# Kernel optimization log

Hardware: AMD Instinct MI355X
Metric: run time of the kernel (lower is better)

## Reference

```python
import jax, jax.numpy as jnp
import numpy as np

B = 65536
L_IN = 1024
DS_FACTOR = 4  # 1024 -> 256 per DownsampleLY so cat gives 512


def fwht(x):
    """Fast Walsh-Hadamard transform over last dim, orthonormal (1/sqrt(n)) scaling."""
    n = x.shape[-1]
    lead = x.shape[:-1]
    h = 1
    while h < n:
        xr = x.reshape(lead + (n // (2 * h), 2, h))
        a = xr[..., 0, :]
        b = xr[..., 1, :]
        x = jnp.stack((a + b, a - b), axis=-2).reshape(lead + (n,))
        h *= 2
    return x * jnp.asarray(1.0 / np.sqrt(n), x.dtype)


def setup_inputs() -> dict:
    key = jax.random.key(0)
    ks = jax.random.split(key, 20)
    s = 0.05  # small init scale for numerical stability
    inp = {
        "x": jax.random.normal(ks[0], (B, L_IN), jnp.float32),
        # learnable downsample taps (factor-4 weighted pooling)
        "dw1": jax.random.normal(ks[1], (DS_FACTOR,), jnp.float32) * 0.25 + 0.25,
        "dw2": jax.random.normal(ks[2], (DS_FACTOR,), jnp.float32) * 0.25 + 0.25,
        # encoder: 512->512->128->64
        "eW1": jax.random.normal(ks[3], (512, 512), jnp.float32) * s,
        "eb1": jnp.zeros((512,), jnp.float32),
        "eW2": jax.random.normal(ks[4], (512, 128), jnp.float32) * s,
        "eb2": jnp.zeros((128,), jnp.float32),
        "eW3": jax.random.normal(ks[5], (128, 64), jnp.float32) * s,
        "eb3": jnp.zeros((64,), jnp.float32),
        # WHT1D channel mix (in=out=1 -> scalar scale + bias)
        "w1c": jnp.ones((), jnp.float32),
        "w1b": jnp.zeros((), jnp.float32),
        # decoder: 64->128->32
        "dW1": jax.random.normal(ks[6], (64, 128), jnp.float32) * s,
        "db1": jnp.zeros((128,), jnp.float32),
        "dW2": jax.random.normal(ks[7], (128, 32), jnp.float32) * s,
        "db2": jnp.zeros((32,), jnp.float32),
        "w2c": jnp.ones((), jnp.float32),
        "w2b": jnp.zeros((), jnp.float32),
        # proj: 32->32
        "pW": jax.random.normal(ks[8], (32, 32), jnp.float32) * s,
        "pb": jnp.zeros((32,), jnp.float32),
    }
    return inp


def reference(x, dw1, dw2, eW1, eb1, eW2, eb2, eW3, eb3, w1c, w1b,
              dW1, db1, dW2, db2, w2c, w2b, pW, pb):
    b = x.shape[0]
    xr = x.reshape(b, L_IN // DS_FACTOR, DS_FACTOR)  # (B, 256, 4)
    R = jnp.einsum('btk,k->bt', xr, dw1)             # (B, 256)
    Z = jnp.einsum('btk,k->bt', xr, dw2)             # (B, 256)
    h = jnp.concatenate((R, Z), axis=1)              # (B, 512)
    # encoder MLP
    h = jax.nn.relu(h @ eW1 + eb1)
    h = jax.nn.relu(h @ eW2 + eb2)
    h = h @ eW3 + eb3                                # (B, 64)
    # WHT1D(64) with 1x1 channel mix
    h = fwht(h) * w1c + w1b
    # decoder MLP
    h = jax.nn.relu(h @ dW1 + db1)
    h = h @ dW2 + db2                                # (B, 32)
    # WHT1D(32)
    h = fwht(h) * w2c + w2b
    # final projection -> (B, 32): [:,:16] real, [:,16:] imag
    return h @ pW + pb
```

## Files before the change

### kernel.cpp

```cpp
#include <hip/hip_runtime.h>

typedef _Float16 f16x8 __attribute__((ext_vector_type(8)));
typedef float f32x4 __attribute__((ext_vector_type(4)));

#define MFMA16(a, b, c) __builtin_amdgcn_mfma_f32_16x16x32_f16(a, b, c, 0, 0, 0)

#define OFF_W1   0u
#define OFF_W2   524288u
#define OFF_W3   655360u
#define OFF_W4   671744u
#define OFF_W5   688128u
#define OFF_W6   696320u
#define OFF_DB1  698368u
#define OFF_PB   698880u

__device__ inline void packw(int local, int N, const float* __restrict__ W,
                             _Float16* __restrict__ dst) {
  int j = local & 7;
  int lane = (local >> 3) & 63;
  int fi = local >> 9;
  int NF = N >> 4;
  int nf = fi % NF;
  int kk = fi / NF;
  int k = kk * 32 + ((lane >> 4) << 3) + j;
  int n = (nf << 4) + (lane & 15);
  dst[local] = (_Float16)W[k * N + n];
}

__device__ inline void packh(int local, int N, int K, const float* __restrict__ W,
                             _Float16* __restrict__ dst, float scale) {
  int j = local & 7;
  int lane = (local >> 3) & 63;
  int fi = local >> 9;
  int NF = N >> 4;
  int nf = fi % NF;
  int kk = fi / NF;
  int k = kk * 32 + ((lane >> 4) << 3) + j;
  int n = (nf << 4) + (lane & 15);
  float s = 0.f;
  for (int m = 0; m < K; ++m) {
    float v = W[m * N + n];
    s += (__popc(k & m) & 1) ? -v : v;
  }
  dst[local] = (_Float16)(s * scale);
}

extern "C" __global__ __launch_bounds__(256) void prep_kernel(
    const float* __restrict__ eW1, const float* __restrict__ eW2,
    const float* __restrict__ eW3, const float* __restrict__ dW1,
    const float* __restrict__ dW2, const float* __restrict__ pW,
    const float* __restrict__ w1c, const float* __restrict__ w1b,
    const float* __restrict__ w2c, const float* __restrict__ w2b,
    const float* __restrict__ db1, const float* __restrict__ pb,
    char* __restrict__ ws) {
  int idx = blockIdx.x * 256 + threadIdx.x;
  if (idx < 262144) {
    packw(idx, 512, eW1, (_Float16*)(ws + OFF_W1));
  } else if (idx < 327680) {
    packw(idx - 262144, 128, eW2, (_Float16*)(ws + OFF_W2));
  } else if (idx < 335872) {
    packw(idx - 327680, 64, eW3, (_Float16*)(ws + OFF_W3));
  } else if (idx < 344064) {
    packh(idx - 335872, 128, 64, dW1, (_Float16*)(ws + OFF_W4), w1c[0] * 0.125f);
  } else if (idx < 348160) {
    packw(idx - 344064, 32, dW2, (_Float16*)(ws + OFF_W5));
  } else if (idx < 349184) {
    packh(idx - 348160, 32, 32, pW, (_Float16*)(ws + OFF_W6),
          w2c[0] * 0.17677669529663687f);
  } else if (idx < 349312) {
    int n = idx - 349184;
    float s = 0.f;
    for (int m = 0; m < 64; ++m) s += dW1[m * 128 + n];
    ((float*)(ws + OFF_DB1))[n] = db1[n] + w1b[0] * s;
  } else if (idx < 349344) {
    int n = idx - 349312;
    float s = 0.f;
    for (int m = 0; m < 32; ++m) s += pW[m * 32 + n];
    ((float*)(ws + OFF_PB))[n] = pb[n] + w2b[0] * s;
  }
}

__device__ inline int hidx(int row, int col, int nu) {
  int u = (col >> 3) ^ ((row & 7) & (nu - 1));
  return row * (nu << 3) + (u << 3) + (col & 7);
}

__device__ inline f16x8 afrag(const _Float16* h, int row, int col, int nu) {
  return *(const f16x8*)(h + hidx(row, col, nu));
}

template <int KK, int NUIN, int NUOUT, bool RELU, int MT>
__device__ inline void layerN(const _Float16* hin, _Float16* hout,
                              const f16x8* __restrict__ Wp,
                              const float* __restrict__ bias, int NFtot, int m0,
                              int nf0, int lane, int g, int rr) {
  f32x4 acc[MT];
#pragma unroll
  for (int m = 0; m < MT; ++m) acc[m] = (f32x4){0.f, 0.f, 0.f, 0.f};
#pragma unroll
  for (int kk = 0; kk < KK; ++kk) {
    f16x8 b = Wp[(kk * NFtot + nf0) * 64 + lane];
#pragma unroll
    for (int m = 0; m < MT; ++m) {
      f16x8 a = afrag(hin, (m0 + m) * 16 + rr, kk * 32 + g * 8, NUIN);
      acc[m] = MFMA16(a, b, acc[m]);
    }
  }
  const int n = nf0 * 16 + rr;
  const float bv = bias[n];
#pragma unroll
  for (int m = 0; m < MT; ++m) {
#pragma unroll
    for (int i = 0; i < 4; ++i) {
      float v = acc[m][i] + bv;
      if (RELU) v = fmaxf(v, 0.f);
      hout[hidx((m0 + m) * 16 + g * 4 + i, n, NUOUT)] = (_Float16)v;
    }
  }
}

#define LDC(C)                                              \
  do {                                                      \
    const float4* p0_ = xrow0 + (C) * 32;                   \
    const float4* p1_ = xrow1 + (C) * 32;                   \
    q0 = p0_[e];  q1 = p0_[e + 8];  q2 = p0_[e + 16];  q3 = p0_[e + 24]; \
    q4 = p1_[e];  q5 = p1_[e + 8];  q6 = p1_[e + 16];  q7 = p1_[e + 24]; \
  } while (0)

#define DOTR(V) (_Float16)((V).x * d10 + (V).y * d11 + (V).z * d12 + (V).w * d13)
#define DOTZ(V) (_Float16)((V).x * d20 + (V).y * d21 + (V).z * d22 + (V).w * d23)

#define CONVQ2(V, ROW, JJ, SR, SZ)                                \
  do {                                                            \
    int ix_ = (ROW) * 32 + ((((JJ) ^ ((ROW) & 3))) << 3) + e;     \
    (SR)[ix_] = DOTR(V);                                          \
    (SZ)[ix_] = DOTZ(V);                                          \
  } while (0)

#define CONVC(SR, SZ)                                             \
  do {                                                            \
    CONVQ2(q0, r8, 0, SR, SZ); CONVQ2(q1, r8, 1, SR, SZ);         \
    CONVQ2(q2, r8, 2, SR, SZ); CONVQ2(q3, r8, 3, SR, SZ);         \
    CONVQ2(q4, r8 + 64, 0, SR, SZ); CONVQ2(q5, r8 + 64, 1, SR, SZ); \
    CONVQ2(q6, r8 + 64, 2, SR, SZ); CONVQ2(q7, r8 + 64, 3, SR, SZ); \
  } while (0)

#define GRID 512

extern "C" __global__ __launch_bounds__(512)
__attribute__((amdgpu_waves_per_eu(2, 2))) void fused_kernel(
    const float* __restrict__ x, const float* __restrict__ dw1,
    const float* __restrict__ dw2, const float* __restrict__ eb1,
    const float* __restrict__ eb2, const float* __restrict__ eb3,
    const float* __restrict__ db2, const char* __restrict__ ws,
    float* __restrict__ out) {
  __shared__ __align__(16) _Float16 LDS[73728];
  _Float16* const h1 = LDS;
  _Float16* const h2 = LDS;
  _Float16* const h4 = LDS + 16384;
  _Float16* const h5 = LDS + 40960;
  _Float16* const h3 = LDS + 65536;
  _Float16* const s0R = LDS + 49152;
  _Float16* const s0Z = LDS + 53248;
  _Float16* const s1R = LDS + 57344;
  _Float16* const s1Z = LDS + 61440;

  const int tid = threadIdx.x;
  const int wg = blockIdx.x;
  const int lane = tid & 63;
  const int w = tid >> 6;
  const int g = lane >> 4;
  const int rr = lane & 15;
  const int r8 = tid >> 3;
  const int e = tid & 7;

  const float d10 = dw1[0], d11 = dw1[1], d12 = dw1[2], d13 = dw1[3];
  const float d20 = dw2[0], d21 = dw2[1], d22 = dw2[2], d23 = dw2[3];

  const f16x8* __restrict__ W1 = (const f16x8*)(ws + OFF_W1);
  const f16x8* __restrict__ W2 = (const f16x8*)(ws + OFF_W2);
  const f16x8* __restrict__ W3 = (const f16x8*)(ws + OFF_W3);
  const f16x8* __restrict__ W4 = (const f16x8*)(ws + OFF_W4);
  const f16x8* __restrict__ W5 = (const f16x8*)(ws + OFF_W5);
  const f16x8* __restrict__ W6 = (const f16x8*)(ws + OFF_W6);
  const float* __restrict__ db1p = (const float*)(ws + OFF_DB1);
  const float* __restrict__ pbp = (const float*)(ws + OFF_PB);

  const float4* __restrict__ xrow0 =
      (const float4*)x + ((size_t)wg * 128 + r8) * 256;
  const float4* __restrict__ xrow1 = xrow0 + (size_t)64 * 256;

  float4 q0, q1, q2, q3, q4, q5, q6, q7;

  LDC(0);
  CONVC(s0R, s0Z);
  __syncthreads();

  f32x4 acc[8][4];
#pragma unroll
  for (int m = 0; m < 8; ++m)
#pragma unroll
    for (int n = 0; n < 4; ++n) acc[m][n] = (f32x4){0.f, 0.f, 0.f, 0.f};

  for (int c = 0; c < 8; ++c) {
    if (c < 7) LDC(c + 1);
    const _Float16* sRp = (c & 1) ? s1R : s0R;
    const _Float16* sZp = (c & 1) ? s1Z : s0Z;
#pragma unroll
    for (int S = 0; S < 2; ++S) {
      const _Float16* sl = S ? sZp : sRp;
      const int kk = S ? (8 + c) : c;
      f16x8 a0 = afrag(sl, rr, g * 8, 4);
      f16x8 a1 = afrag(sl, 16 + rr, g * 8, 4);
      f16x8 a2 = afrag(sl, 32 + rr, g * 8, 4);
      f16x8 a3 = afrag(sl, 48 + rr, g * 8, 4);
      f16x8 a4 = afrag(sl, 64 + rr, g * 8, 4);
      f16x8 a5 = afrag(sl, 80 + rr, g * 8, 4);
      f16x8 a6 = afrag(sl, 96 + rr, g * 8, 4);
      f16x8 a7 = afrag(sl, 112 + rr, g * 8, 4);
#pragma unroll
      for (int nf = 0; nf < 4; ++nf) {
        f16x8 bb = W1[(kk * 32 + w * 4 + nf) * 64 + lane];
        acc[0][nf] = MFMA16(a0, bb, acc[0][nf]);
        acc[1][nf] = MFMA16(a1, bb, acc[1][nf]);
        acc[2][nf] = MFMA16(a2, bb, acc[2][nf]);
        acc[3][nf] = MFMA16(a3, bb, acc[3][nf]);
        acc[4][nf] = MFMA16(a4, bb, acc[4][nf]);
        acc[5][nf] = MFMA16(a5, bb, acc[5][nf]);
        acc[6][nf] = MFMA16(a6, bb, acc[6][nf]);
        acc[7][nf] = MFMA16(a7, bb, acc[7][nf]);
      }
    }
    if (c < 7) {
      _Float16* dR = (c & 1) ? s0R : s1R;
      _Float16* dZ = (c & 1) ? s0Z : s1Z;
      CONVC(dR, dZ);
    }
    __syncthreads();
  }

#pragma unroll
  for (int mt = 0; mt < 8; ++mt) {
#pragma unroll
    for (int nf = 0; nf < 4; ++nf) {
      const int n = (w * 4 + nf) * 16 + rr;
      const float bv = eb1[n];
#pragma unroll
      for (int i = 0; i < 4; ++i) {
        float v = fmaxf(acc[mt][nf][i] + bv, 0.f);
        h1[hidx(mt * 16 + g * 4 + i, n, 64)] = (_Float16)v;
      }
    }
  }
  __syncthreads();

  {
    f32x4 acc2[8];
#pragma unroll
    for (int m = 0; m < 8; ++m) acc2[m] = (f32x4){0.f, 0.f, 0.f, 0.f};
#pragma unroll
    for (int kk = 0; kk < 16; ++kk) {
      f16x8 b2 = W2[(kk * 8 + w) * 64 + lane];
#pragma unroll
      for (int m = 0; m < 8; ++m) {
        f16x8 a = afrag(h1, m * 16 + rr, kk * 32 + g * 8, 64);
        acc2[m] = MFMA16(a, b2, acc2[m]);
      }
    }
    const float bv2 = eb2[w * 16 + rr];
    __syncthreads();
#pragma unroll
    for (int m = 0; m < 8; ++m) {
#pragma unroll
      for (int i = 0; i < 4; ++i) {
        float v = fmaxf(acc2[m][i] + bv2, 0.f);
        h2[hidx(m * 16 + g * 4 + i, w * 16 + rr, 16)] = (_Float16)v;
      }
    }
  }
  __syncthreads();

  layerN<4, 16, 8, false, 4>(h2, h3, W3, eb3, 4, (w >> 2) * 4, w & 3, lane, g, rr);
  __syncthreads();
  layerN<2, 8, 16, true, 8>(h3, h4, W4, db1p, 8, 0, w, lane, g, rr);
  __syncthreads();
  layerN<4, 16, 4, false, 2>(h4, h5, W5, db2, 2, (w >> 1) * 2, w & 1, lane, g, rr);
  __syncthreads();

  {
    const int m5 = (w >> 1) * 2;
    const int nf5 = w & 1;
    const int n = nf5 * 16 + rr;
    const float bv6 = pbp[n];
    f16x8 b6 = W6[nf5 * 64 + lane];
#pragma unroll
    for (int m = 0; m < 2; ++m) {
      f16x8 a = afrag(h5, (m5 + m) * 16 + rr, g * 8, 4);
      f32x4 o = MFMA16(a, b6, ((f32x4){0.f, 0.f, 0.f, 0.f}));
      const size_t rbase = (size_t)wg * 128 + (m5 + m) * 16;
#pragma unroll
      for (int i = 0; i < 4; ++i) {
        out[(rbase + g * 4 + i) * 32 + n] = o[i] + bv6;
      }
    }
  }
}

extern "C" void kernel_launch(void* const* d_in, const int* in_sizes, int n_in,
                              void* d_out, int out_size, void* d_ws, size_t ws_size,
                              hipStream_t stream) {
  const float* x = (const float*)d_in[0];
  const float* dw1 = (const float*)d_in[1];
  const float* dw2 = (const float*)d_in[2];
  const float* eW1 = (const float*)d_in[3];
  const float* eb1 = (const float*)d_in[4];
  const float* eW2 = (const float*)d_in[5];
  const float* eb2 = (const float*)d_in[6];
  const float* eW3 = (const float*)d_in[7];
  const float* eb3 = (const float*)d_in[8];
  const float* w1c = (const float*)d_in[9];
  const float* w1b = (const float*)d_in[10];
  const float* dW1 = (const float*)d_in[11];
  const float* db1 = (const float*)d_in[12];
  const float* dW2 = (const float*)d_in[13];
  const float* db2 = (const float*)d_in[14];
  const float* w2c = (const float*)d_in[15];
  const float* w2b = (const float*)d_in[16];
  const float* pW = (const float*)d_in[17];
  const float* pb = (const float*)d_in[18];
  char* ws = (char*)d_ws;
  float* out = (float*)d_out;

  prep_kernel<<<dim3(1365), dim3(256), 0, stream>>>(eW1, eW2, eW3, dW1, dW2, pW, w1c, w1b,
                                                    w2c, w2b, db1, pb, ws);
  fused_kernel<<<dim3(GRID), dim3(512), 0, stream>>>(x, dw1, dw2, eb1, eb2, eb3, db2, ws,
                                                     out);
}
```

Before: 79.74 us.

## Process two row blocks per workgroup and prefetch next block's first chunk

Halves the grid so each workgroup handles two 128-row blocks in sequence. The first x chunk of the next block is loaded and converted into the stage-0 LDS buffer during the tail layers of the current block, overlapping global loads with the small MLP layers. This trades grid parallelism (256 workgroups on 256 CUs) for hiding the initial load latency, and adds LDS aliasing risk between s0R/s0Z and the h buffers.

```diff
diff --git a/kernel.cpp b/kernel.cpp
--- a/kernel.cpp
+++ b/kernel.cpp
@@ -119,10 +119,10 @@
   }
 }
 
-#define LDC(C)                                              \
+#define LDCG(P0, P1, C)                                     \
   do {                                                      \
-    const float4* p0_ = xrow0 + (C) * 32;                   \
-    const float4* p1_ = xrow1 + (C) * 32;                   \
+    const float4* p0_ = (P0) + (C) * 32;                    \
+    const float4* p1_ = (P1) + (C) * 32;                    \
     q0 = p0_[e];  q1 = p0_[e + 8];  q2 = p0_[e + 16];  q3 = p0_[e + 24]; \
     q4 = p1_[e];  q5 = p1_[e + 8];  q6 = p1_[e + 16];  q7 = p1_[e + 24]; \
   } while (0)
@@ -145,7 +145,8 @@
     CONVQ2(q6, r8 + 64, 2, SR, SZ); CONVQ2(q7, r8 + 64, 3, SR, SZ); \
   } while (0)
 
-#define GRID 512
+#define NB 2
+#define GRID 256
 
 extern "C" __global__ __launch_bounds__(512)
 __attribute__((amdgpu_waves_per_eu(2, 2))) void fused_kernel(
@@ -186,121 +187,136 @@
   const float* __restrict__ db1p = (const float*)(ws + OFF_DB1);
   const float* __restrict__ pbp = (const float*)(ws + OFF_PB);
 
-  const float4* __restrict__ xrow0 =
-      (const float4*)x + ((size_t)wg * 128 + r8) * 256;
-  const float4* __restrict__ xrow1 = xrow0 + (size_t)64 * 256;
-
   float4 q0, q1, q2, q3, q4, q5, q6, q7;
 
-  LDC(0);
-  CONVC(s0R, s0Z);
+  {
+    const float4* __restrict__ p0 = (const float4*)x + ((size_t)wg * 128 + r8) * 256;
+    const float4* __restrict__ p1 = p0 + (size_t)64 * 256;
+    LDCG(p0, p1, 0);
+    CONVC(s0R, s0Z);
+  }
   __syncthreads();
 
-  f32x4 acc[8][4];
-#pragma unroll
-  for (int m = 0; m < 8; ++m)
-#pragma unroll
-    for (int n = 0; n < 4; ++n) acc[m][n] = (f32x4){0.f, 0.f, 0.f, 0.f};
-
-  for (int c = 0; c < 8; ++c) {
-    if (c < 7) LDC(c + 1);
-    const _Float16* sRp = (c & 1) ? s1R : s0R;
-    const _Float16* sZp = (c & 1) ? s1Z : s0Z;
-#pragma unroll
-    for (int S = 0; S < 2; ++S) {
-      const _Float16* sl = S ? sZp : sRp;
-      const int kk = S ? (8 + c) : c;
-      f16x8 a0 = afrag(sl, rr, g * 8, 4);
-      f16x8 a1 = afrag(sl, 16 + rr, g * 8, 4);
-      f16x8 a2 = afrag(sl, 32 + rr, g * 8, 4);
-      f16x8 a3 = afrag(sl, 48 + rr, g * 8, 4);
-      f16x8 a4 = afrag(sl, 64 + rr, g * 8, 4);
-      f16x8 a5 = afrag(sl, 80 + rr, g * 8, 4);
-      f16x8 a6 = afrag(sl, 96 + rr, g * 8, 4);
-      f16x8 a7 = afrag(sl, 112 + rr, g * 8, 4);
+  for (int b = 0; b < NB; ++b) {
+    const size_t blkIdx = (size_t)wg + (size_t)GRID * b;
+    const float4* __restrict__ xrow0 = (const float4*)x + (blkIdx * 128 + r8) * 256;
+    const float4* __restrict__ xrow1 = xrow0 + (size_t)64 * 256;
+    const bool stage = (b + 1 < NB);
+
+    f32x4 acc[8][4];
+#pragma unroll
+    for (int m = 0; m < 8; ++m)
+#pragma unroll
+      for (int n = 0; n < 4; ++n) acc[m][n] = (f32x4){0.f, 0.f, 0.f, 0.f};
+
+    for (int c = 0; c < 8; ++c) {
+      if (c < 7) LDCG(xrow0, xrow1, c + 1);
+      const _Float16* sRp = (c & 1) ? s1R : s0R;
+      const _Float16* sZp = (c & 1) ? s1Z : s0Z;
+#pragma unroll
+      for (int S = 0; S < 2; ++S) {
+        const _Float16* sl = S ? sZp : sRp;
+        const int kk = S ? (8 + c) : c;
+        f16x8 a0 = afrag(sl, rr, g * 8, 4);
+        f16x8 a1 = afrag(sl, 16 + rr, g * 8, 4);
+        f16x8 a2 = afrag(sl, 32 + rr, g * 8, 4);
+        f16x8 a3 = afrag(sl, 48 + rr, g * 8, 4);
+        f16x8 a4 = afrag(sl, 64 + rr, g * 8, 4);
+        f16x8 a5 = afrag(sl, 80 + rr, g * 8, 4);
+        f16x8 a6 = afrag(sl, 96 + rr, g * 8, 4);
+        f16x8 a7 = afrag(sl, 112 + rr, g * 8, 4);
+#pragma unroll
+        for (int nf = 0; nf < 4; ++nf) {
+          f16x8 bb = W1[(kk * 32 + w * 4 + nf) * 64 + lane];
+          acc[0][nf] = MFMA16(a0, bb, acc[0][nf]);
+          acc[1][nf] = MFMA16(a1, bb, acc[1][nf]);
+          acc[2][nf] = MFMA16(a2, bb, acc[2][nf]);
+          acc[3][nf] = MFMA16(a3, bb, acc[3][nf]);
+          acc[4][nf] = MFMA16(a4, bb, acc[4][nf]);
+          acc[5][nf] = MFMA16(a5, bb, acc[5][nf]);
+          acc[6][nf] = MFMA16(a6, bb, acc[6][nf]);
+          acc[7][nf] = MFMA16(a7, bb, acc[7][nf]);
+        }
+      }
+      if (c < 7) {
+        _Float16* dR = (c & 1) ? s0R : s1R;
+        _Float16* dZ = (c & 1) ? s0Z : s1Z;
+        CONVC(dR, dZ);
+      }
+      __syncthreads();
+    }
+
+#pragma unroll
+    for (int mt = 0; mt < 8; ++mt) {
 #pragma unroll
       for (int nf = 0; nf < 4; ++nf) {
-        f16x8 bb = W1[(kk * 32 + w * 4 + nf) * 64 + lane];
-        acc[0][nf] = MFMA16(a0, bb, acc[0][nf]);
-        acc[1][nf] = MFMA16(a1, bb, acc[1][nf]);
-        acc[2][nf] = MFMA16(a2, bb, acc[2][nf]);
-        acc[3][nf] = MFMA16(a3, bb, acc[3][nf]);
-        acc[4][nf] = MFMA16(a4, bb, acc[4][nf]);
-        acc[5][nf] = MFMA16(a5, bb, acc[5][nf]);
-        acc[6][nf] = MFMA16(a6, bb, acc[6][nf]);
-        acc[7][nf] = MFMA16(a7, bb, acc[7][nf]);
-      }
-    }
-    if (c < 7) {
-      _Float16* dR = (c & 1) ? s0R : s1R;
-      _Float16* dZ = (c & 1) ? s0Z : s1Z;
-      CONVC(dR, dZ);
-    }
-    __syncthreads();
-  }
-
-#pragma unroll
-  for (int mt = 0; mt < 8; ++mt) {
-#pragma unroll
-    for (int nf = 0; nf < 4; ++nf) {
-      const int n = (w * 4 + nf) * 16 + rr;
-      const float bv = eb1[n];
-#pragma unroll
-      for (int i = 0; i < 4; ++i) {
-        float v = fmaxf(acc[mt][nf][i] + bv, 0.f);
-        h1[hidx(mt * 16 + g * 4 + i, n, 64)] = (_Float16)v;
-      }
-    }
-  }
-  __syncthreads();
-
-  {
-    f32x4 acc2[8];
-#pragma unroll
-    for (int m = 0; m < 8; ++m) acc2[m] = (f32x4){0.f, 0.f, 0.f, 0.f};
-#pragma unroll
-    for (int kk = 0; kk < 16; ++kk) {
-      f16x8 b2 = W2[(kk * 8 + w) * 64 + lane];
+        const int n = (w * 4 + nf) * 16 + rr;
+        const float bv = eb1[n];
+#pragma unroll
+        for (int i = 0; i < 4; ++i) {
+          float v = fmaxf(acc[mt][nf][i] + bv, 0.f);
+          h1[hidx(mt * 16 + g * 4 + i, n, 64)] = (_Float16)v;
+        }
+      }
+    }
+    __syncthreads();
+
+    {
+      f32x4 acc2[8];
+#pragma unroll
+      for (int m = 0; m < 8; ++m) acc2[m] = (f32x4){0.f, 0.f, 0.f, 0.f};
+#pragma unroll
+      for (int kk = 0; kk < 16; ++kk) {
+        f16x8 b2 = W2[(kk * 8 + w) * 64 + lane];
+#pragma unroll
+        for (int m = 0; m < 8; ++m) {
+          f16x8 a = afrag(h1, m * 16 + rr, kk * 32 + g * 8, 64);
+          acc2[m] = MFMA16(a, b2, acc2[m]);
+        }
+      }
+      const float bv2 = eb2[w * 16 + rr];
+      __syncthreads();
 #pragma unroll
       for (int m = 0; m < 8; ++m) {
-        f16x8 a = afrag(h1, m * 16 + rr, kk * 32 + g * 8, 64);
-        acc2[m] = MFMA16(a, b2, acc2[m]);
-      }
-    }
-    const float bv2 = eb2[w * 16 + rr];
-    __syncthreads();
-#pragma unroll
-    for (int m = 0; m < 8; ++m) {
-#pragma unroll
-      for (int i = 0; i < 4; ++i) {
-        float v = fmaxf(acc2[m][i] + bv2, 0.f);
-        h2[hidx(m * 16 + g * 4 + i, w * 16 + rr, 16)] = (_Float16)v;
-      }
-    }
-  }
-  __syncthreads();
-
-  layerN<4, 16, 8, false, 4>(h2, h3, W3, eb3, 4, (w >> 2) * 4, w & 3, lane, g, rr);
-  __syncthreads();
-  layerN<2, 8, 16, true, 8>(h3, h4, W4, db1p, 8, 0, w, lane, g, rr);
-  __syncthreads();
-  layerN<4, 16, 4, false, 2>(h4, h5, W5, db2, 2, (w >> 1) * 2, w & 1, lane, g, rr);
-  __syncthreads();
-
-  {
-    const int m5 = (w >> 1) * 2;
-    const int nf5 = w & 1;
-    const int n = nf5 * 16 + rr;
-    const float bv6 = pbp[n];
-    f16x8 b6 = W6[nf5 * 64 + lane];
-#pragma unroll
-    for (int m = 0; m < 2; ++m) {
-      f16x8 a = afrag(h5, (m5 + m) * 16 + rr, g * 8, 4);
-      f32x4 o = MFMA16(a, b6, ((f32x4){0.f, 0.f, 0.f, 0.f}));
-      const size_t rbase = (size_t)wg * 128 + (m5 + m) * 16;
-#pragma unroll
-      for (int i = 0; i < 4; ++i) {
-        out[(rbase + g * 4 + i) * 32 + n] = o[i] + bv6;
+#pragma unroll
+        for (int i = 0; i < 4; ++i) {
+          float v = fmaxf(acc2[m][i] + bv2, 0.f);
+          h2[hidx(m * 16 + g * 4 + i, w * 16 + rr, 16)] = (_Float16)v;
+        }
+      }
+    }
+    __syncthreads();
+
+    if (stage) {
+      const float4* __restrict__ xn0 =
+          (const float4*)x + (((size_t)wg + (size_t)GRID * (b + 1)) * 128 + r8) * 256;
+      const float4* __restrict__ xn1 = xn0 + (size_t)64 * 256;
+      LDCG(xn0, xn1, 0);
+      CONVC(s0R, s0Z);
+    }
+
+    layerN<4, 16, 8, false, 4>(h2, h3, W3, eb3, 4, (w >> 2) * 4, w & 3, lane, g, rr);
+    __syncthreads();
+    layerN<2, 8, 16, true, 8>(h3, h4, W4, db1p, 8, 0, w, lane, g, rr);
+    __syncthreads();
+    layerN<4, 16, 4, false, 2>(h4, h5, W5, db2, 2, (w >> 1) * 2, w & 1, lane, g, rr);
+    __syncthreads();
+
+    {
+      const int m5 = (w >> 1) * 2;
+      const int nf5 = w & 1;
+      const int n = nf5 * 16 + rr;
+      const float bv6 = pbp[n];
+      f16x8 b6 = W6[nf5 * 64 + lane];
+#pragma unroll
+      for (int m = 0; m < 2; ++m) {
+        f16x8 a = afrag(h5, (m5 + m) * 16 + rr, g * 8, 4);
+        f32x4 o = MFMA16(a, b6, ((f32x4){0.f, 0.f, 0.f, 0.f}));
+        const size_t rbase = blkIdx * 128 + (m5 + m) * 16;
+#pragma unroll
+        for (int i = 0; i < 4; ++i) {
+          out[(rbase + g * 4 + i) * 32 + n] = o[i] + bv6;
+        }
       }
     }
   }
```

Measured after the change: 305.8 us. +283.5%, slower.
